# Kernel optimization log

Measured on AMD Instinct MI355X. Metric: run time of the kernel, lower is better.

Reference implementation:

```python
import jax, jax.numpy as jnp
import numpy as np
import math

# ---- cfg constants (PUMA functional model defaults) ----
XBAR_ROW, XBAR_COL = 128, 128
GON, GOFF, VMAX = 1.0 / 100.0, 1.0 / 600.0, 0.25  # cancel exactly in ideal ADC decode
BIT_SLICE, BIT_STREAM = 2, 1
WEIGHT_BITS, INPUT_BITS = 16, 16
W_FRAC = WEIGHT_BITS // 4 * 3   # 12 fractional bits (default -1 path)
I_FRAC = INPUT_BITS // 4 * 3    # 12
ACM_BITS = 16
ACM_FRAC = ACM_BITS // 4 * 3    # 12 -> accumulator range [-8, 8)
ADC_BIT = int(math.log2(XBAR_ROW)) + BIT_SLICE  # 7 + 2 = 9 (bit_stream==1 adds nothing)
NSLICE = 2 ** BIT_SLICE - 1     # conductance states per slice
NS = WEIGHT_BITS // BIT_SLICE   # 8 weight slices, MSB first
NB = INPUT_BITS // BIT_STREAM   # 16 input bit streams, LSB first


def bit_slicing(w):
    # w: [out, in] nonnegative -> [in, out*NS]; per output col, NS slices MSB first
    wint = jnp.clip(jnp.round(w * 2.0 ** W_FRAC), 0.0, 2.0 ** WEIGHT_BITS - 1)
    shifts = 2.0 ** (BIT_SLICE * jnp.arange(NS - 1, -1, -1, dtype=jnp.float32))
    sl = jnp.floor(wint[:, :, None] / shifts) % (2 ** BIT_SLICE)  # [out,in,NS]
    return sl.transpose(1, 0, 2).reshape(w.shape[1], w.shape[0] * NS)


def to_bits(x):
    # two's-complement fixed-point bits, LSB first -> [B, in, NB]
    xint = jnp.clip(jnp.round(x * 2.0 ** I_FRAC), -(2.0 ** (INPUT_BITS - 1)), 2.0 ** (INPUT_BITS - 1) - 1)
    xint = jnp.where(xint < 0, xint + 2.0 ** INPUT_BITS, xint)
    shifts = 2.0 ** jnp.arange(INPUT_BITS, dtype=jnp.float32)
    return jnp.floor(xint[:, :, None] / shifts) % 2.0


def tile(ws, rt, ct):
    # pad [rows, cols] to crossbar tiles [rt, ct, XBAR_ROW, XBAR_COL]
    pad = jnp.zeros((rt * XBAR_ROW, ct * XBAR_COL), ws.dtype)
    pad = pad.at[:ws.shape[0], :ws.shape[1]].set(ws)
    return pad.reshape(rt, XBAR_ROW, ct, XBAR_COL).transpose(0, 2, 1, 3)


def quant_acm(v):
    lim = 2.0 ** (ACM_BITS - ACM_FRAC - 1)
    q = jnp.round(v * 2.0 ** ACM_FRAC) / 2.0 ** ACM_FRAC
    return jnp.clip(q, -lim, lim - 2.0 ** (-ACM_FRAC))


def crossbar_mvm(bits, slices):
    # bits: [B, R, 128, NB] in {0,1}; slices: [R, C, 128, 128] in {0..NSLICE}
    G = slices * (GON - GOFF) / NSLICE + GOFF          # conductance mapping
    V = bits * VMAX                                     # DAC (1-bit streams)
    # analog column currents per stream: [B, R, C, NB, 128]
    I = jnp.einsum('brks,rckj->brcsj', V, G)
    vsum = V.sum(2)                                     # [B, R, NB]
    # ideal decode: remove Goff offset, rescale to integer dot counts
    counts = (I - vsum[:, :, None, :, None] * GOFF) / (VMAX * (GON - GOFF) / NSLICE)
    # ADC quantization over full-scale range xbar_row*NSLICE with 2**ADC_BIT levels
    step = (XBAR_ROW * NSLICE) / (2.0 ** ADC_BIT - 1)
    counts = jnp.round(counts / step) * step
    B, R, C = counts.shape[:3]
    counts = counts.reshape(B, R, C, NB, XBAR_COL // NS, NS)
    slice_w = 2.0 ** (BIT_SLICE * jnp.arange(NS - 1, -1, -1, dtype=jnp.float32))
    psum = (counts * slice_w).sum(-1)                   # shift-add slices -> [B,R,C,NB,cols]
    stream_w = 2.0 ** jnp.arange(NB, dtype=jnp.float32)
    stream_w = stream_w.at[-1].multiply(-1.0)           # two's-complement MSB is negative
    out = (psum * stream_w[:, None]).sum(3)             # shift-add streams -> [B,R,C,cols]
    out = quant_acm(out / 2.0 ** (W_FRAC + I_FRAC))     # back to float, accumulator quant
    out = out.sum(1)                                    # digital sum over row tiles
    return out.reshape(B, C * (XBAR_COL // NS))


def mvm_forward(x, weight):
    out_f, in_f = weight.shape
    pos = bit_slicing(jnp.clip(weight, 0.0, None))
    neg = bit_slicing(jnp.abs(jnp.clip(weight, None, 0.0)))
    rt = -(-pos.shape[0] // XBAR_ROW)
    ct = -(-pos.shape[1] // XBAR_COL)
    xb_pos, xb_neg = tile(pos, rt, ct), tile(neg, rt, ct)
    bits = to_bits(x)                                   # [B, in, NB]
    B = x.shape[0]
    bits_p = jnp.zeros((B, rt * XBAR_ROW, NB), x.dtype).at[:, :in_f].set(bits)
    bits_p = bits_p.reshape(B, rt, XBAR_ROW, NB)
    out = crossbar_mvm(bits_p, xb_pos) - crossbar_mvm(bits_p, xb_neg)
    return out[:, :out_f]


def setup_inputs() -> dict:
    key = jax.random.key(0)
    k1, k2, k3 = jax.random.split(key, 3)
    x = jax.random.normal(k1, (512, 1024), dtype=jnp.float32) * 0.1
    weight = jax.random.normal(k2, (128, 1024), dtype=jnp.float32) * 0.05
    bias = jax.random.uniform(k3, (128,), dtype=jnp.float32, minval=-0.1, maxval=0.1)
    return {"x": x, "weight": weight, "bias": bias}


def reference(x, weight, bias):
    return mvm_forward(x, weight) + bias[None, :]
```

## Files before the change

### kernel.cpp

```cpp
#include <hip/hip_runtime.h>
#include <stdint.h>

typedef __attribute__((ext_vector_type(4)))  int i32x4;
typedef __attribute__((ext_vector_type(16))) int i32x16;

#define XM_OFF 0u
#define BP_OFF 1048576u
#define PT_OFF 3145728u

__device__ __forceinline__ uint32_t q16(float v){
  float f = fminf(fmaxf(rintf(v*4096.f), -32768.f), 32767.f);
  return (uint32_t)(int)f & 0xffffu;
}

__global__ __launch_bounds__(256) void pack_k(const float* __restrict__ x, const float* __restrict__ w,
                                              uint4* __restrict__ xm, uint32_t* __restrict__ Bw){
  const int lane = threadIdx.x & 63;
  if (blockIdx.x < 1024){
    int wv = blockIdx.x*4 + (threadIdx.x >> 6);
    int b = wv >> 3, z = wv & 7;
    const float* xp = x + b*1024 + z*128;
    uint32_t u0 = q16(xp[lane]);
    uint32_t u1 = q16(xp[lane + 64]);
    uint4 out4 = {0,0,0,0};
    #pragma unroll
    for (int s = 0; s < 16; ++s){
      unsigned long long m0 = __ballot((u0 >> s) & 1u);
      unsigned long long m1 = __ballot((u1 >> s) & 1u);
      if (lane == s){
        out4.x = (uint32_t)m0; out4.y = (uint32_t)(m0 >> 32);
        out4.z = (uint32_t)m1; out4.w = (uint32_t)(m1 >> 32);
      }
    }
    if (lane < 16) xm[(b*8 + z)*16 + lane] = out4;
  } else {
    int t = (blockIdx.x - 1024)*256 + threadIdx.x;
    int j = t >> 8, kq = t & 255;
    int r = kq >> 5, kd = kq & 31;
    float4 v = *reinterpret_cast<const float4*>(w + j*1024 + kq*4);
    #pragma unroll
    for (int p = 0; p < 2; ++p){
      uint32_t q0 = (uint32_t)fminf(rintf(fmaxf(p ? -v.x : v.x, 0.f)*4096.f), 65535.f);
      uint32_t q1 = (uint32_t)fminf(rintf(fmaxf(p ? -v.y : v.y, 0.f)*4096.f), 65535.f);
      uint32_t q2 = (uint32_t)fminf(rintf(fmaxf(p ? -v.z : v.z, 0.f)*4096.f), 65535.f);
      uint32_t q3 = (uint32_t)fminf(rintf(fmaxf(p ? -v.w : v.w, 0.f)*4096.f), 65535.f);
      #pragma unroll
      for (int sl = 0; sl < 8; ++sl){
        int sh = 2*(7 - sl);
        uint32_t word = ((q0 >> sh) & 3u) | (((q1 >> sh) & 3u) << 8)
                      | (((q2 >> sh) & 3u) << 16) | (((q3 >> sh) & 3u) << 24);
        Bw[(((r*2 + p)*8 + sl)*128 + j)*32 + kd] = word;
      }
    }
  }
}

__global__ __launch_bounds__(512) void mvm_main_k(const uint4* __restrict__ xm,
                                                  const uint8_t* __restrict__ Bp,
                                                  float* __restrict__ partial){
  __shared__ uint8_t lds[65536];
  __shared__ uint32_t flg[8];
  const int tid = threadIdx.x, lane = tid & 63, wid = tid >> 6;
  const int z = blockIdx.z, jblk = blockIdx.y;
  const int col = lane & 31, hi = lane >> 5;

  {
    const int q = lane >> 3, cS = (lane & 7) ^ q;
    uint32_t f2 = 0;
    #pragma unroll
    for (int u = 0; u < 2; ++u){
      const int si = wid + u*8;
      const uint8_t* src = Bp + ((size_t)((z*16 + si)*128 + jblk*32) << 7);
      uint4 r0 = *(const uint4*)(src + (q     )*128 + cS*16);
      uint4 r1 = *(const uint4*)(src + (q +  8)*128 + cS*16);
      uint4 r2 = *(const uint4*)(src + (q + 16)*128 + cS*16);
      uint4 r3 = *(const uint4*)(src + (q + 24)*128 + cS*16);
      uint8_t* dst = lds + si*4096 + lane*16;
      *(uint4*)(dst       ) = r0;
      *(uint4*)(dst + 1024) = r1;
      *(uint4*)(dst + 2048) = r2;
      *(uint4*)(dst + 3072) = r3;
      uint32_t o = r0.x|r0.y|r0.z|r0.w | r1.x|r1.y|r1.z|r1.w
                 | r2.x|r2.y|r2.z|r2.w | r3.x|r3.y|r3.z|r3.w;
      f2 |= (__any(o != 0u) ? 1u : 0u) << u;
    }
    if (lane == 0) flg[wid] = f2;
  }

  const int b_w = blockIdx.x*16 + wid*2;
  const int b_a = b_w + (col >> 4);
  const int s_a = lane & 15;
  const uint4 pw = xm[(b_a*8 + z)*16 + s_a];
  i32x4 afr[4];
  {
    const uint32_t wd[4] = {pw.x, pw.y, pw.z, pw.w};
    #pragma unroll
    for (int f = 0; f < 4; ++f){
      uint32_t pl = wd[f] >> (hi*16);
      #pragma unroll
      for (int wI = 0; wI < 4; ++wI)
        afr[f][wI] = (int)((((pl >> (wI*4)) & 0xFu) * 0x204081u) & 0x01010101u);
    }
  }
  __syncthreads();

  uint32_t msk = 0;
  #pragma unroll
  for (int w2 = 0; w2 < 8; ++w2){
    uint32_t f2 = flg[w2];
    msk |= (f2 & 1u) << w2;
    msk |= ((f2 >> 1) & 1u) << (w2 + 8);
  }
  msk = __builtin_amdgcn_readfirstlane(msk);

  const int c7 = col & 7;
  const int xo0 = ((0 + hi) ^ c7) << 4;
  const int xo1 = ((2 + hi) ^ c7) << 4;
  const int xo2 = ((4 + hi) ^ c7) << 4;
  const int xo3 = ((6 + hi) ^ c7) << 4;

  i32x16 zz;
  #pragma unroll
  for (int i = 0; i < 16; ++i) zz[i] = 0;

  const float C1 = (float)(511.0/384.0);
  const float QC = (float)(384.0/511.0/4096.0);
  const float sc  = hi ? 16.0f : 1.0f;
  const float w11 = hi ? -32768.0f : 2048.0f;
  float out0 = 0.f, out1 = 0.f;

  #pragma unroll
  for (int ph = 0; ph < 2; ++ph){
    float vacc[16];
    #pragma unroll
    for (int g = 0; g < 16; ++g) vacc[g] = 0.f;

    #pragma unroll
    for (int sl = 0; sl < 8; ++sl){
      const int ti = ph*8 + sl;
      if (msk & (1u << ti)){
        const uint8_t* lb = lds + ti*4096 + col*128;
        i32x4 b0 = *(const i32x4*)(lb + xo0);
        i32x4 b1 = *(const i32x4*)(lb + xo1);
        i32x4 b2 = *(const i32x4*)(lb + xo2);
        i32x4 b3 = *(const i32x4*)(lb + xo3);
        i32x16 cc = zz;
        cc = __builtin_amdgcn_mfma_i32_32x32x32_i8(afr[0], b0, cc, 0, 0, 0);
        cc = __builtin_amdgcn_mfma_i32_32x32x32_i8(afr[1], b1, cc, 0, 0, 0);
        cc = __builtin_amdgcn_mfma_i32_32x32x32_i8(afr[2], b2, cc, 0, 0, 0);
        cc = __builtin_amdgcn_mfma_i32_32x32x32_i8(afr[3], b3, cc, 0, 0, 0);
        const float slw = (float)(1 << (14 - 2*sl));
        #pragma unroll
        for (int g = 0; g < 16; ++g)
          vacc[g] = fmaf(rintf((float)cc[g] * C1), slw, vacc[g]);
      }
    }

    float a0 = 0.f, a1 = 0.f;
    #pragma unroll
    for (int g = 0; g < 7; ++g){
      const int s_lo = (g & 3) + 8*((g >> 2) & 1);
      a0 = fmaf(vacc[g],     (float)(1 << s_lo), a0);
      a1 = fmaf(vacc[g + 8], (float)(1 << s_lo), a1);
    }
    a0 = fmaf(vacc[7],  w11, a0*sc);
    a1 = fmaf(vacc[15], w11, a1*sc);
    a0 += __shfl_xor(a0, 32);
    a1 += __shfl_xor(a1, 32);

    float q0 = rintf(a0 * QC) * (1.0f/4096.0f);
    q0 = fminf(fmaxf(q0, -8.0f), 8.0f - 1.0f/4096.0f);
    float q1 = rintf(a1 * QC) * (1.0f/4096.0f);
    q1 = fminf(fmaxf(q1, -8.0f), 8.0f - 1.0f/4096.0f);
    if (ph == 0){ out0 += q0; out1 += q1; } else { out0 -= q0; out1 -= q1; }
  }

  const int jout = jblk*32 + col;
  partial[(z*512 + b_w + hi)*128 + jout] = hi ? out1 : out0;
}

__global__ __launch_bounds__(256) void reduce_k(const float* __restrict__ partial,
                                                const float* __restrict__ bias,
                                                float* __restrict__ out){
  int t = blockIdx.x*256 + threadIdx.x;
  int b = t >> 7, j = t & 127;
  float s = 0.f;
  #pragma unroll
  for (int z = 0; z < 8; ++z) s += partial[(z*512 + b)*128 + j];
  out[t] = s + bias[j];
}

extern "C" void kernel_launch(void* const* d_in, const int* in_sizes, int n_in,
                              void* d_out, int out_size, void* d_ws, size_t ws_size,
                              hipStream_t stream){
  const float* x    = (const float*)d_in[0];
  const float* w    = (const float*)d_in[1];
  const float* bias = (const float*)d_in[2];
  uint8_t* ws = (uint8_t*)d_ws;

  hipLaunchKernelGGL(pack_k, dim3(1152), dim3(256), 0, stream,
                     x, w, (uint4*)(ws + XM_OFF), (uint32_t*)(ws + BP_OFF));
  hipLaunchKernelGGL(mvm_main_k, dim3(32, 4, 8), dim3(512), 0, stream,
                     (const uint4*)(ws + XM_OFF), ws + BP_OFF, (float*)(ws + PT_OFF));
  hipLaunchKernelGGL(reduce_k, dim3(256), dim3(256), 0, stream,
                     (const float*)(ws + PT_OFF), bias, (float*)d_out);
}
```

Baseline: 28.07 us.

## Precompute slice-nonzero masks in pack kernel and pipeline MFMA over active slices

The pack kernel now builds a per-(row-tile, column-block) bitmask of nonzero weight slices with wave shuffles and atomicOr into a workspace buffer. The main kernel reads this mask up front, skips global loads of all-zero slices, and drops the LDS flag exchange. It also compacts the active slice list and double-buffers two MFMA accumulators, so one slice's epilogue overlaps the next slice's matrix ops, with raised priority around the MFMAs. The cost is an extra memset launch, atomics in the pack kernel, and higher register pressure from the occupancy hint and two accumulators.

```diff
diff --git a/kernel.cpp b/kernel.cpp
--- a/kernel.cpp
+++ b/kernel.cpp
@@ -6,7 +6,8 @@
 
 #define XM_OFF 0u
 #define BP_OFF 1048576u
-#define PT_OFF 3145728u
+#define MK_OFF 3145728u
+#define PT_OFF 3149824u
 
 __device__ __forceinline__ uint32_t q16(float v){
   float f = fminf(fmaxf(rintf(v*4096.f), -32768.f), 32767.f);
@@ -14,7 +15,8 @@
 }
 
 __global__ __launch_bounds__(256) void pack_k(const float* __restrict__ x, const float* __restrict__ w,
-                                              uint4* __restrict__ xm, uint32_t* __restrict__ Bw){
+                                              uint4* __restrict__ xm, uint32_t* __restrict__ Bw,
+                                              uint32_t* __restrict__ mask){
   const int lane = threadIdx.x & 63;
   if (blockIdx.x < 1024){
     int wv = blockIdx.x*4 + (threadIdx.x >> 6);
@@ -38,6 +40,7 @@
     int j = t >> 8, kq = t & 255;
     int r = kq >> 5, kd = kq & 31;
     float4 v = *reinterpret_cast<const float4*>(w + j*1024 + kq*4);
+    uint32_t lm = 0;
     #pragma unroll
     for (int p = 0; p < 2; ++p){
       uint32_t q0 = (uint32_t)fminf(rintf(fmaxf(p ? -v.x : v.x, 0.f)*4096.f), 65535.f);
@@ -50,41 +53,47 @@
         uint32_t word = ((q0 >> sh) & 3u) | (((q1 >> sh) & 3u) << 8)
                       | (((q2 >> sh) & 3u) << 16) | (((q3 >> sh) & 3u) << 24);
         Bw[(((r*2 + p)*8 + sl)*128 + j)*32 + kd] = word;
-      }
-    }
-  }
-}
-
-__global__ __launch_bounds__(512) void mvm_main_k(const uint4* __restrict__ xm,
-                                                  const uint8_t* __restrict__ Bp,
-                                                  float* __restrict__ partial){
+        lm |= (word != 0u ? 1u : 0u) << (p*8 + sl);
+      }
+    }
+    lm |= (uint32_t)__shfl_xor((int)lm, 16);
+    lm |= (uint32_t)__shfl_xor((int)lm, 8);
+    lm |= (uint32_t)__shfl_xor((int)lm, 4);
+    lm |= (uint32_t)__shfl_xor((int)lm, 2);
+    lm |= (uint32_t)__shfl_xor((int)lm, 1);
+    if ((threadIdx.x & 31) == 0) atomicOr(&mask[r*4 + (j >> 5)], lm);
+  }
+}
+
+__global__ __launch_bounds__(512, 4) void mvm_main_k(const uint4* __restrict__ xm,
+                                                     const uint8_t* __restrict__ Bp,
+                                                     const uint32_t* __restrict__ mask,
+                                                     float* __restrict__ partial){
   __shared__ uint8_t lds[65536];
-  __shared__ uint32_t flg[8];
   const int tid = threadIdx.x, lane = tid & 63, wid = tid >> 6;
   const int z = blockIdx.z, jblk = blockIdx.y;
   const int col = lane & 31, hi = lane >> 5;
 
+  const uint32_t msk = (uint32_t)__builtin_amdgcn_readfirstlane((int)(mask[z*4 + jblk] & 0xFFFFu));
+
   {
     const int q = lane >> 3, cS = (lane & 7) ^ q;
-    uint32_t f2 = 0;
     #pragma unroll
     for (int u = 0; u < 2; ++u){
       const int si = wid + u*8;
-      const uint8_t* src = Bp + ((size_t)((z*16 + si)*128 + jblk*32) << 7);
-      uint4 r0 = *(const uint4*)(src + (q     )*128 + cS*16);
-      uint4 r1 = *(const uint4*)(src + (q +  8)*128 + cS*16);
-      uint4 r2 = *(const uint4*)(src + (q + 16)*128 + cS*16);
-      uint4 r3 = *(const uint4*)(src + (q + 24)*128 + cS*16);
-      uint8_t* dst = lds + si*4096 + lane*16;
-      *(uint4*)(dst       ) = r0;
-      *(uint4*)(dst + 1024) = r1;
-      *(uint4*)(dst + 2048) = r2;
-      *(uint4*)(dst + 3072) = r3;
-      uint32_t o = r0.x|r0.y|r0.z|r0.w | r1.x|r1.y|r1.z|r1.w
-                 | r2.x|r2.y|r2.z|r2.w | r3.x|r3.y|r3.z|r3.w;
-      f2 |= (__any(o != 0u) ? 1u : 0u) << u;
-    }
-    if (lane == 0) flg[wid] = f2;
+      if (msk & (1u << si)){
+        const uint8_t* src = Bp + ((size_t)((z*16 + si)*128 + jblk*32) << 7);
+        uint4 r0 = *(const uint4*)(src + (q     )*128 + cS*16);
+        uint4 r1 = *(const uint4*)(src + (q +  8)*128 + cS*16);
+        uint4 r2 = *(const uint4*)(src + (q + 16)*128 + cS*16);
+        uint4 r3 = *(const uint4*)(src + (q + 24)*128 + cS*16);
+        uint8_t* dst = lds + si*4096 + lane*16;
+        *(uint4*)(dst       ) = r0;
+        *(uint4*)(dst + 1024) = r1;
+        *(uint4*)(dst + 2048) = r2;
+        *(uint4*)(dst + 3072) = r3;
+      }
+    }
   }
 
   const int b_w = blockIdx.x*16 + wid*2;
@@ -104,15 +113,6 @@
   }
   __syncthreads();
 
-  uint32_t msk = 0;
-  #pragma unroll
-  for (int w2 = 0; w2 < 8; ++w2){
-    uint32_t f2 = flg[w2];
-    msk |= (f2 & 1u) << w2;
-    msk |= ((f2 >> 1) & 1u) << (w2 + 8);
-  }
-  msk = __builtin_amdgcn_readfirstlane(msk);
-
   const int c7 = col & 7;
   const int xo0 = ((0 + hi) ^ c7) << 4;
   const int xo1 = ((2 + hi) ^ c7) << 4;
@@ -129,30 +129,57 @@
   const float w11 = hi ? -32768.0f : 2048.0f;
   float out0 = 0.f, out1 = 0.f;
 
+#define MFMA4(cc, lbp) do { \
+    const uint8_t* lb_ = (lbp); \
+    i32x4 b0_ = *(const i32x4*)(lb_ + xo0); \
+    i32x4 b1_ = *(const i32x4*)(lb_ + xo1); \
+    i32x4 b2_ = *(const i32x4*)(lb_ + xo2); \
+    i32x4 b3_ = *(const i32x4*)(lb_ + xo3); \
+    __builtin_amdgcn_s_setprio(1); \
+    cc = __builtin_amdgcn_mfma_i32_32x32x32_i8(afr[0], b0_, zz, 0, 0, 0); \
+    cc = __builtin_amdgcn_mfma_i32_32x32x32_i8(afr[1], b1_, cc, 0, 0, 0); \
+    cc = __builtin_amdgcn_mfma_i32_32x32x32_i8(afr[2], b2_, cc, 0, 0, 0); \
+    cc = __builtin_amdgcn_mfma_i32_32x32x32_i8(afr[3], b3_, cc, 0, 0, 0); \
+    __builtin_amdgcn_s_setprio(0); \
+  } while (0)
+
+#define EPI(cc, slw) do { \
+    _Pragma("unroll") \
+    for (int g_ = 0; g_ < 16; ++g_) \
+      vacc[g_] = fmaf(rintf((float)cc[g_] * C1), (slw), vacc[g_]); \
+  } while (0)
+
   #pragma unroll
-  for (int ph = 0; ph < 2; ++ph){
+  for (int p = 0; p < 2; ++p){
+    const uint32_t m = (msk >> (p*8)) & 0xFFu;
     float vacc[16];
     #pragma unroll
     for (int g = 0; g < 16; ++g) vacc[g] = 0.f;
 
-    #pragma unroll
-    for (int sl = 0; sl < 8; ++sl){
-      const int ti = ph*8 + sl;
-      if (msk & (1u << ti)){
-        const uint8_t* lb = lds + ti*4096 + col*128;
-        i32x4 b0 = *(const i32x4*)(lb + xo0);
-        i32x4 b1 = *(const i32x4*)(lb + xo1);
-        i32x4 b2 = *(const i32x4*)(lb + xo2);
-        i32x4 b3 = *(const i32x4*)(lb + xo3);
-        i32x16 cc = zz;
-        cc = __builtin_amdgcn_mfma_i32_32x32x32_i8(afr[0], b0, cc, 0, 0, 0);
-        cc = __builtin_amdgcn_mfma_i32_32x32x32_i8(afr[1], b1, cc, 0, 0, 0);
-        cc = __builtin_amdgcn_mfma_i32_32x32x32_i8(afr[2], b2, cc, 0, 0, 0);
-        cc = __builtin_amdgcn_mfma_i32_32x32x32_i8(afr[3], b3, cc, 0, 0, 0);
-        const float slw = (float)(1 << (14 - 2*sl));
-        #pragma unroll
-        for (int g = 0; g < 16; ++g)
-          vacc[g] = fmaf(rintf((float)cc[g] * C1), slw, vacc[g]);
+    if (m){
+      uint32_t lst = 0; int nr = 0;
+      uint32_t mm = m;
+      while (mm){ lst |= (uint32_t)(__ffs(mm) - 1) << (4*nr); mm &= mm - 1; ++nr; }
+      int n = nr;
+      if (n & 1){ lst |= (lst & 15u) << (4*n); ++n; }
+
+      const uint8_t* base = lds + (p*8)*4096 + col*128;
+      i32x16 ccA, ccB;
+      const int slA0 = (int)(lst & 15u);
+      MFMA4(ccA, base + slA0*4096);
+      float slwA = (float)(1 << (14 - 2*slA0));
+      int t = 0;
+      while (true){
+        const int slB = (int)((lst >> (4*t + 4)) & 15u);
+        MFMA4(ccB, base + slB*4096);
+        const float slwB = (t + 1 < nr) ? (float)(1 << (14 - 2*slB)) : 0.0f;
+        EPI(ccA, slwA);
+        if (t + 2 >= n){ EPI(ccB, slwB); break; }
+        const int slA = (int)((lst >> (4*t + 8)) & 15u);
+        MFMA4(ccA, base + slA*4096);
+        slwA = (float)(1 << (14 - 2*slA));
+        EPI(ccB, slwB);
+        t += 2;
       }
     }
 
@@ -172,8 +199,11 @@
     q0 = fminf(fmaxf(q0, -8.0f), 8.0f - 1.0f/4096.0f);
     float q1 = rintf(a1 * QC) * (1.0f/4096.0f);
     q1 = fminf(fmaxf(q1, -8.0f), 8.0f - 1.0f/4096.0f);
-    if (ph == 0){ out0 += q0; out1 += q1; } else { out0 -= q0; out1 -= q1; }
-  }
+    if (p == 0){ out0 += q0; out1 += q1; } else { out0 -= q0; out1 -= q1; }
+  }
+
+#undef MFMA4
+#undef EPI
 
   const int jout = jblk*32 + col;
   partial[(z*512 + b_w + hi)*128 + jout] = hi ? out1 : out0;
@@ -198,10 +228,12 @@
   const float* bias = (const float*)d_in[2];
   uint8_t* ws = (uint8_t*)d_ws;
 
+  hipMemsetAsync(ws + MK_OFF, 0, 128, stream);
   hipLaunchKernelGGL(pack_k, dim3(1152), dim3(256), 0, stream,
-                     x, w, (uint4*)(ws + XM_OFF), (uint32_t*)(ws + BP_OFF));
+                     x, w, (uint4*)(ws + XM_OFF), (uint32_t*)(ws + BP_OFF), (uint32_t*)(ws + MK_OFF));
   hipLaunchKernelGGL(mvm_main_k, dim3(32, 4, 8), dim3(512), 0, stream,
-                     (const uint4*)(ws + XM_OFF), ws + BP_OFF, (float*)(ws + PT_OFF));
+                     (const uint4*)(ws + XM_OFF), ws + BP_OFF,
+                     (const uint32_t*)(ws + MK_OFF), (float*)(ws + PT_OFF));
   hipLaunchKernelGGL(reduce_k, dim3(256), dim3(256), 0, stream,
                      (const float*)(ws + PT_OFF), bias, (float*)d_out);
 }
```

Result: slower. 36.83 us (+31.2%).

## Process two batch groups per wave to reuse LDS weight tiles and halve grid

Applied to the files above, without the earlier changes.

Each wave now handles four batch rows (two A-fragment sets) against the same LDS-staged weight slices, so each block covers twice the batch and the grid's x-dimension halves. This halves the global-to-LDS weight staging per output. The per-slice epilogue is also restructured to fold the slice and bit-weight scaling into two scalar accumulators instead of a 16-entry vacc array. The cost is more registers and fewer blocks (512 instead of 1024) to fill the GPU.

```diff
diff --git a/kernel.cpp b/kernel.cpp
--- a/kernel.cpp
+++ b/kernel.cpp
@@ -55,9 +55,9 @@
   }
 }
 
-__global__ __launch_bounds__(512) void mvm_main_k(const uint4* __restrict__ xm,
-                                                  const uint8_t* __restrict__ Bp,
-                                                  float* __restrict__ partial){
+__global__ __launch_bounds__(512, 4) void mvm_main_k(const uint4* __restrict__ xm,
+                                                     const uint8_t* __restrict__ Bp,
+                                                     float* __restrict__ partial){
   __shared__ uint8_t lds[65536];
   __shared__ uint32_t flg[8];
   const int tid = threadIdx.x, lane = tid & 63, wid = tid >> 6;
@@ -87,19 +87,23 @@
     if (lane == 0) flg[wid] = f2;
   }
 
-  const int b_w = blockIdx.x*16 + wid*2;
-  const int b_a = b_w + (col >> 4);
+  const int bb  = blockIdx.x*32 + wid*4;
   const int s_a = lane & 15;
-  const uint4 pw = xm[(b_a*8 + z)*16 + s_a];
-  i32x4 afr[4];
+  const uint4 pwA = xm[((bb     + (col >> 4))*8 + z)*16 + s_a];
+  const uint4 pwB = xm[((bb + 2 + (col >> 4))*8 + z)*16 + s_a];
+  i32x4 afrA[4], afrB[4];
   {
-    const uint32_t wd[4] = {pw.x, pw.y, pw.z, pw.w};
+    const uint32_t wA[4] = {pwA.x, pwA.y, pwA.z, pwA.w};
+    const uint32_t wB[4] = {pwB.x, pwB.y, pwB.z, pwB.w};
     #pragma unroll
     for (int f = 0; f < 4; ++f){
-      uint32_t pl = wd[f] >> (hi*16);
+      uint32_t plA = wA[f] >> (hi*16);
+      uint32_t plB = wB[f] >> (hi*16);
       #pragma unroll
-      for (int wI = 0; wI < 4; ++wI)
-        afr[f][wI] = (int)((((pl >> (wI*4)) & 0xFu) * 0x204081u) & 0x01010101u);
+      for (int wI = 0; wI < 4; ++wI){
+        afrA[f][wI] = (int)((((plA >> (wI*4)) & 0xFu) * 0x204081u) & 0x01010101u);
+        afrB[f][wI] = (int)((((plB >> (wI*4)) & 0xFu) * 0x204081u) & 0x01010101u);
+      }
     }
   }
   __syncthreads();
@@ -111,7 +115,7 @@
     msk |= (f2 & 1u) << w2;
     msk |= ((f2 >> 1) & 1u) << (w2 + 8);
   }
-  msk = __builtin_amdgcn_readfirstlane(msk);
+  msk = (uint32_t)__builtin_amdgcn_readfirstlane((int)msk);
 
   const int c7 = col & 7;
   const int xo0 = ((0 + hi) ^ c7) << 4;
@@ -125,58 +129,65 @@
 
   const float C1 = (float)(511.0/384.0);
   const float QC = (float)(384.0/511.0/4096.0);
-  const float sc  = hi ? 16.0f : 1.0f;
-  const float w11 = hi ? -32768.0f : 2048.0f;
-  float out0 = 0.f, out1 = 0.f;
-
-  #pragma unroll
-  for (int ph = 0; ph < 2; ++ph){
-    float vacc[16];
-    #pragma unroll
-    for (int g = 0; g < 16; ++g) vacc[g] = 0.f;
-
+  const float sc = hi ? 16.0f : 1.0f;
+  const float w7 = hi ? -8.0f : 8.0f;
+  float oA0 = 0.f, oA1 = 0.f, oB0 = 0.f, oB1 = 0.f;
+
+#define EPI(cc, A0, A1) do { \
+    float nf[16]; \
+    _Pragma("unroll") \
+    for (int g_ = 0; g_ < 16; ++g_) nf[g_] = rintf((float)cc[g_] * C1); \
+    float t0 = fmaf(nf[1], 2.f, nf[0]);  t0 = fmaf(nf[2], 4.f, t0);  t0 = fmaf(nf[3], 8.f, t0); \
+    float t1 = fmaf(nf[5], 2.f, nf[4]);  t1 = fmaf(nf[6], 4.f, t1);  t1 = fmaf(nf[7], w7, t1); \
+    float t2 = fmaf(nf[9], 2.f, nf[8]);  t2 = fmaf(nf[10],4.f, t2);  t2 = fmaf(nf[11],8.f, t2); \
+    float t3 = fmaf(nf[13],2.f, nf[12]); t3 = fmaf(nf[14],4.f, t3);  t3 = fmaf(nf[15],w7, t3); \
+    A0 = fmaf(t0, slwv, A0);  A0 = fmaf(t1, slw256, A0); \
+    A1 = fmaf(t2, slwv, A1);  A1 = fmaf(t3, slw256, A1); \
+  } while (0)
+
+  #pragma unroll
+  for (int p = 0; p < 2; ++p){
+    float aA0 = 0.f, aA1 = 0.f, aB0 = 0.f, aB1 = 0.f;
     #pragma unroll
     for (int sl = 0; sl < 8; ++sl){
-      const int ti = ph*8 + sl;
+      const int ti = p*8 + sl;
       if (msk & (1u << ti)){
+        const float slwv   = (float)(1 << (14 - 2*sl));
+        const float slw256 = slwv * 256.0f;
         const uint8_t* lb = lds + ti*4096 + col*128;
         i32x4 b0 = *(const i32x4*)(lb + xo0);
         i32x4 b1 = *(const i32x4*)(lb + xo1);
         i32x4 b2 = *(const i32x4*)(lb + xo2);
         i32x4 b3 = *(const i32x4*)(lb + xo3);
-        i32x16 cc = zz;
-        cc = __builtin_amdgcn_mfma_i32_32x32x32_i8(afr[0], b0, cc, 0, 0, 0);
-        cc = __builtin_amdgcn_mfma_i32_32x32x32_i8(afr[1], b1, cc, 0, 0, 0);
-        cc = __builtin_amdgcn_mfma_i32_32x32x32_i8(afr[2], b2, cc, 0, 0, 0);
-        cc = __builtin_amdgcn_mfma_i32_32x32x32_i8(afr[3], b3, cc, 0, 0, 0);
-        const float slw = (float)(1 << (14 - 2*sl));
-        #pragma unroll
-        for (int g = 0; g < 16; ++g)
-          vacc[g] = fmaf(rintf((float)cc[g] * C1), slw, vacc[g]);
-      }
-    }
-
-    float a0 = 0.f, a1 = 0.f;
-    #pragma unroll
-    for (int g = 0; g < 7; ++g){
-      const int s_lo = (g & 3) + 8*((g >> 2) & 1);
-      a0 = fmaf(vacc[g],     (float)(1 << s_lo), a0);
-      a1 = fmaf(vacc[g + 8], (float)(1 << s_lo), a1);
-    }
-    a0 = fmaf(vacc[7],  w11, a0*sc);
-    a1 = fmaf(vacc[15], w11, a1*sc);
-    a0 += __shfl_xor(a0, 32);
-    a1 += __shfl_xor(a1, 32);
-
-    float q0 = rintf(a0 * QC) * (1.0f/4096.0f);
-    q0 = fminf(fmaxf(q0, -8.0f), 8.0f - 1.0f/4096.0f);
-    float q1 = rintf(a1 * QC) * (1.0f/4096.0f);
-    q1 = fminf(fmaxf(q1, -8.0f), 8.0f - 1.0f/4096.0f);
-    if (ph == 0){ out0 += q0; out1 += q1; } else { out0 -= q0; out1 -= q1; }
-  }
+        i32x16 cc = __builtin_amdgcn_mfma_i32_32x32x32_i8(afrA[0], b0, zz, 0, 0, 0);
+        cc = __builtin_amdgcn_mfma_i32_32x32x32_i8(afrA[1], b1, cc, 0, 0, 0);
+        cc = __builtin_amdgcn_mfma_i32_32x32x32_i8(afrA[2], b2, cc, 0, 0, 0);
+        cc = __builtin_amdgcn_mfma_i32_32x32x32_i8(afrA[3], b3, cc, 0, 0, 0);
+        i32x16 cd = __builtin_amdgcn_mfma_i32_32x32x32_i8(afrB[0], b0, zz, 0, 0, 0);
+        cd = __builtin_amdgcn_mfma_i32_32x32x32_i8(afrB[1], b1, cd, 0, 0, 0);
+        cd = __builtin_amdgcn_mfma_i32_32x32x32_i8(afrB[2], b2, cd, 0, 0, 0);
+        cd = __builtin_amdgcn_mfma_i32_32x32x32_i8(afrB[3], b3, cd, 0, 0, 0);
+        EPI(cc, aA0, aA1);
+        EPI(cd, aB0, aB1);
+      }
+    }
+
+    aA0 *= sc; aA1 *= sc; aB0 *= sc; aB1 *= sc;
+    aA0 += __shfl_xor(aA0, 32); aA1 += __shfl_xor(aA1, 32);
+    aB0 += __shfl_xor(aB0, 32); aB1 += __shfl_xor(aB1, 32);
+
+    float qA0 = fminf(fmaxf(rintf(aA0*QC)*(1.0f/4096.0f), -8.0f), 8.0f - 1.0f/4096.0f);
+    float qA1 = fminf(fmaxf(rintf(aA1*QC)*(1.0f/4096.0f), -8.0f), 8.0f - 1.0f/4096.0f);
+    float qB0 = fminf(fmaxf(rintf(aB0*QC)*(1.0f/4096.0f), -8.0f), 8.0f - 1.0f/4096.0f);
+    float qB1 = fminf(fmaxf(rintf(aB1*QC)*(1.0f/4096.0f), -8.0f), 8.0f - 1.0f/4096.0f);
+    if (p == 0){ oA0 += qA0; oA1 += qA1; oB0 += qB0; oB1 += qB1; }
+    else       { oA0 -= qA0; oA1 -= qA1; oB0 -= qB0; oB1 -= qB1; }
+  }
+#undef EPI
 
   const int jout = jblk*32 + col;
-  partial[(z*512 + b_w + hi)*128 + jout] = hi ? out1 : out0;
+  partial[(z*512 + bb + hi    )*128 + jout] = hi ? oA1 : oA0;
+  partial[(z*512 + bb + 2 + hi)*128 + jout] = hi ? oB1 : oB0;
 }
 
 __global__ __launch_bounds__(256) void reduce_k(const float* __restrict__ partial,
@@ -200,7 +211,7 @@
 
   hipLaunchKernelGGL(pack_k, dim3(1152), dim3(256), 0, stream,
                      x, w, (uint4*)(ws + XM_OFF), (uint32_t*)(ws + BP_OFF));
-  hipLaunchKernelGGL(mvm_main_k, dim3(32, 4, 8), dim3(512), 0, stream,
+  hipLaunchKernelGGL(mvm_main_k, dim3(16, 4, 8), dim3(512), 0, stream,
                      (const uint4*)(ws + XM_OFF), ws + BP_OFF, (float*)(ws + PT_OFF));
   hipLaunchKernelGGL(reduce_k, dim3(256), dim3(256), 0, stream,
                      (const float*)(ws + PT_OFF), bias, (float*)d_out);
```

Measured after the change: 26.93 us. 1.04x faster.
